# Performance work log

Measured on AMD Instinct MI355X. Metric: run time of the kernel, lower is better.

## Reference

```python
import jax, jax.numpy as jnp
import numpy as np
import math

B, S_TGT, S_SRC, D, H, FF = 4, 2048, 2048, 512, 8, 2048
DK = D // H
EPS = 1e-6


def layernorm(x, gamma, mu):
    # torch: gamma*(x-mean)/(std+eps)+mu with unbiased std (ddof=1), eps OUTSIDE sqrt
    mean = jnp.mean(x, axis=-1, keepdims=True)
    std = jnp.std(x, axis=-1, keepdims=True, ddof=1)
    return gamma * (x - mean) / (std + EPS) + mu


def mha(q, k, v, wq, wk, wv, wo, bo, mask):
    # q:[B,Sq,D] k,v:[B,Sk,D]; weights [D,D] (applied as x@W)
    Bq, Sq, _ = q.shape
    Sk = k.shape[1]
    Q = (q @ wq).reshape(Bq, Sq, H, DK).transpose(0, 2, 1, 3)  # [B,H,Sq,dk]
    K = (k @ wk).reshape(Bq, Sk, H, DK).transpose(0, 2, 1, 3)
    V = (v @ wv).reshape(Bq, Sk, H, DK).transpose(0, 2, 1, 3)
    scores = jnp.einsum('bhqd,bhkd->bhqk', Q, K) / math.sqrt(DK)
    scores = jnp.where(mask == 0, -1e9, scores)
    attn = jax.nn.softmax(scores, axis=-1)
    out = jnp.einsum('bhqk,bhkd->bhqd', attn, V)  # [B,H,Sq,dk]
    out = out.transpose(0, 2, 1, 3).reshape(Bq, Sq, D)
    return out @ wo + bo


def setup_inputs() -> dict:
    key = jax.random.key(0)
    ks = jax.random.split(key, 20)
    sc = 0.02
    inp = {
        'x': jax.random.normal(ks[0], (B, S_TGT, D), jnp.float32),
        'encoder_output': jax.random.normal(ks[1], (B, S_SRC, D), jnp.float32),
        'src_mask': jnp.ones((1, 1, 1, S_SRC), jnp.int32),
        'tgt_mask': jnp.tril(jnp.ones((S_TGT, S_TGT), jnp.int32))[None, None],
        # self-attention params
        'sa_wq': jax.random.normal(ks[2], (D, D)) * sc,
        'sa_wk': jax.random.normal(ks[3], (D, D)) * sc,
        'sa_wv': jax.random.normal(ks[4], (D, D)) * sc,
        'sa_wo': jax.random.normal(ks[5], (D, D)) * sc,
        'sa_bo': jnp.zeros((D,), jnp.float32),
        # cross-attention params
        'ca_wq': jax.random.normal(ks[6], (D, D)) * sc,
        'ca_wk': jax.random.normal(ks[7], (D, D)) * sc,
        'ca_wv': jax.random.normal(ks[8], (D, D)) * sc,
        'ca_wo': jax.random.normal(ks[9], (D, D)) * sc,
        'ca_bo': jnp.zeros((D,), jnp.float32),
        # feed-forward params
        'ff_w1': jax.random.normal(ks[10], (D, FF)) * sc,
        'ff_b1': jnp.zeros((FF,), jnp.float32),
        'ff_w2': jax.random.normal(ks[11], (FF, D)) * sc,
        'ff_b2': jnp.zeros((D,), jnp.float32),
        # layernorm params (3 residual connections)
        'ln0_g': jnp.ones((D,), jnp.float32), 'ln0_b': jnp.zeros((D,), jnp.float32),
        'ln1_g': jnp.ones((D,), jnp.float32), 'ln1_b': jnp.zeros((D,), jnp.float32),
        'ln2_g': jnp.ones((D,), jnp.float32), 'ln2_b': jnp.zeros((D,), jnp.float32),
    }
    return inp


def reference(x, encoder_output, src_mask, tgt_mask,
              sa_wq, sa_wk, sa_wv, sa_wo, sa_bo,
              ca_wq, ca_wk, ca_wv, ca_wo, ca_bo,
              ff_w1, ff_b1, ff_w2, ff_b2,
              ln0_g, ln0_b, ln1_g, ln1_b, ln2_g, ln2_b):
    # pre-LN residual blocks; dropout in eval mode (identity)
    h = layernorm(x, ln0_g, ln0_b)
    x = x + mha(h, h, h, sa_wq, sa_wk, sa_wv, sa_wo, sa_bo, tgt_mask)
    h = layernorm(x, ln1_g, ln1_b)
    x = x + mha(h, encoder_output, encoder_output, ca_wq, ca_wk, ca_wv, ca_wo, ca_bo, src_mask)
    h = layernorm(x, ln2_g, ln2_b)
    ff = jax.nn.relu(h @ ff_w1 + ff_b1) @ ff_w2 + ff_b2
    return x + ff
```

## Files before the change

### kernel.cpp

```cpp
#include <hip/hip_runtime.h>
#include <cstdint>

typedef short s8v __attribute__((ext_vector_type(8)));
typedef short s4v __attribute__((ext_vector_type(4)));
typedef float f4v __attribute__((ext_vector_type(4)));
typedef unsigned int u32;

#define DEV static __device__ __forceinline__

DEV unsigned short f2bf(float f) {
  u32 u = __builtin_bit_cast(u32, f);
  u += 0x7FFF + ((u >> 16) & 1);
  return (unsigned short)(u >> 16);
}

DEV void gload16(const void* g, void* l) {
  __builtin_amdgcn_global_load_lds(
      (const __attribute__((address_space(1))) u32*)g,
      (__attribute__((address_space(3))) u32*)l, 16, 0, 0);
}

struct TransArgs {
  const float* in[10];
  unsigned short* out[10];
};

__global__ __launch_bounds__(256) void trans_all_kernel(TransArgs ta) {
  int id = blockIdx.x;
  int wi, t, K, N, tx, ty;
  if (id < 2048) {
    wi = id >> 8; t = id & 255; K = 512; N = 512; tx = t & 15; ty = t >> 4;
  } else if (id < 3072) {
    wi = 8; t = id - 2048; K = 512; N = 2048; tx = t & 63; ty = t >> 6;
  } else {
    wi = 9; t = id - 3072; K = 2048; N = 512; tx = t & 15; ty = t >> 4;
  }
  const float* in = ta.in[wi];
  unsigned short* out = ta.out[wi];
  __shared__ float tile[32][33];
  int lx = threadIdx.x & 31, ly = threadIdx.x >> 5;
  int bn = tx * 32, bk = ty * 32;
#pragma unroll
  for (int i = 0; i < 32; i += 8)
    tile[ly + i][lx] = in[(size_t)(bk + ly + i) * N + bn + lx];
  __syncthreads();
#pragma unroll
  for (int i = 0; i < 32; i += 8)
    out[(size_t)(bn + ly + i) * K + bk + lx] = f2bf(tile[lx][ly + i]);
}

__global__ __launch_bounds__(256) void cast_kernel(
    const float* __restrict__ in, unsigned short* __restrict__ out, int n8) {
  int i = blockIdx.x * 256 + threadIdx.x;
  if (i >= n8) return;
  const float4* p = (const float4*)(in + (size_t)i * 8);
  float4 a = p[0], b = p[1];
  float va[8] = {a.x, a.y, a.z, a.w, b.x, b.y, b.z, b.w};
  s8v o;
#pragma unroll
  for (int j = 0; j < 8; j++) o[j] = (short)f2bf(va[j]);
  *(s8v*)(out + (size_t)i * 8) = o;
}

__global__ __launch_bounds__(256) void ln_kernel(
    const float* __restrict__ x, const float* __restrict__ g,
    const float* __restrict__ bt, unsigned short* __restrict__ out) {
  int row = blockIdx.x * 4 + (threadIdx.x >> 6);
  int lane = threadIdx.x & 63;
  const float* xr = x + (size_t)row * 512 + lane * 8;
  float4 v0 = *(const float4*)xr;
  float4 v1 = *(const float4*)(xr + 4);
  float va[8] = {v0.x, v0.y, v0.z, v0.w, v1.x, v1.y, v1.z, v1.w};
  float s = 0.f, s2 = 0.f;
#pragma unroll
  for (int j = 0; j < 8; j++) { s += va[j]; s2 += va[j] * va[j]; }
#pragma unroll
  for (int off = 1; off < 64; off <<= 1) {
    s += __shfl_xor(s, off);
    s2 += __shfl_xor(s2, off);
  }
  float mean = s * (1.f / 512.f);
  float var = (s2 - 512.f * mean * mean) * (1.f / 511.f);
  var = fmaxf(var, 0.f);
  float inv = 1.f / (sqrtf(var) + 1e-6f);
  const float* gp = g + lane * 8;
  const float* bp = bt + lane * 8;
  float4 g0 = *(const float4*)gp, g1 = *(const float4*)(gp + 4);
  float4 b0 = *(const float4*)bp, b1 = *(const float4*)(bp + 4);
  float ga[8] = {g0.x, g0.y, g0.z, g0.w, g1.x, g1.y, g1.z, g1.w};
  float ba[8] = {b0.x, b0.y, b0.z, b0.w, b1.x, b1.y, b1.z, b1.w};
  s8v o;
#pragma unroll
  for (int j = 0; j < 8; j++)
    o[j] = (short)f2bf(ga[j] * (va[j] - mean) * inv + ba[j]);
  *(s8v*)(out + (size_t)row * 512 + lane * 8) = o;
}

#define EPI_QKV3 0
#define EPI_Q 1
#define EPI_KV2 2
#define EPI_BIAS_RES 3
#define EPI_RELU 4

template <int EPI>
__global__ __launch_bounds__(256) void gemm_kernel(
    const unsigned short* __restrict__ A, const unsigned short* __restrict__ Bt,
    const float* __restrict__ bias, const float* __restrict__ res,
    void* __restrict__ out0, void* __restrict__ out1, void* __restrict__ out2,
    int M, int N, int K) {
  __shared__ alignas(16) unsigned short sA[128 * 32];
  __shared__ alignas(16) unsigned short sB[128 * 32];
  int tid = threadIdx.x;
  int w = tid >> 6, lane = tid & 63;
  int wm = w >> 1, wn = w & 1;
  int quad = lane >> 4, l15 = lane & 15;
  int bm = blockIdx.y * 128, bn = blockIdx.x * 128;

  int r0 = lane >> 2, c0 = (lane & 3) * 8;
  const unsigned short* gA0 = A + (size_t)(bm + w * 16 + r0) * K + c0;
  const unsigned short* gA1 = gA0 + (size_t)64 * K;
  const unsigned short* gB0 = Bt + (size_t)(bn + w * 16 + r0) * K + c0;
  const unsigned short* gB1 = gB0 + (size_t)64 * K;
  unsigned short* lA0 = &sA[(w * 64 + lane) * 8];
  unsigned short* lA1 = &sA[((w + 4) * 64 + lane) * 8];
  unsigned short* lB0 = &sB[(w * 64 + lane) * 8];
  unsigned short* lB1 = &sB[((w + 4) * 64 + lane) * 8];

  f4v acc[4][4];
#pragma unroll
  for (int r = 0; r < 4; r++)
#pragma unroll
    for (int c = 0; c < 4; c++) acc[r][c] = {0.f, 0.f, 0.f, 0.f};

  for (int k0 = 0; k0 < K; k0 += 32) {
    gload16(gA0 + k0, lA0);
    gload16(gA1 + k0, lA1);
    gload16(gB0 + k0, lB0);
    gload16(gB1 + k0, lB1);
    __syncthreads();
    s8v af[4], bf[4];
#pragma unroll
    for (int r = 0; r < 4; r++)
      af[r] = *(const s8v*)&sA[(wm * 64 + r * 16 + l15) * 32 + quad * 8];
#pragma unroll
    for (int c = 0; c < 4; c++)
      bf[c] = *(const s8v*)&sB[(wn * 64 + c * 16 + l15) * 32 + quad * 8];
#pragma unroll
    for (int r = 0; r < 4; r++)
#pragma unroll
      for (int c = 0; c < 4; c++)
        acc[r][c] = __builtin_amdgcn_mfma_f32_16x16x32_bf16(af[r], bf[c], acc[r][c], 0, 0, 0);
    __syncthreads();
  }

  int route = 0;
  if (EPI == EPI_QKV3) route = blockIdx.x >> 2;
  if (EPI == EPI_KV2) route = 1 + (blockIdx.x >> 2);
#pragma unroll
  for (int r = 0; r < 4; r++) {
#pragma unroll
    for (int c = 0; c < 4; c++) {
#pragma unroll
      for (int i = 0; i < 4; i++) {
        int row = bm + wm * 64 + r * 16 + quad * 4 + i;
        int col = bn + wn * 64 + c * 16 + l15;
        float v = acc[r][c][i];
        if (EPI == EPI_BIAS_RES) {
          float* o = (float*)out0;
          o[(size_t)row * N + col] = v + bias[col] + res[(size_t)row * N + col];
        } else if (EPI == EPI_RELU) {
          unsigned short* o = (unsigned short*)out0;
          o[(size_t)row * N + col] = f2bf(fmaxf(v + bias[col], 0.f));
        } else {
          int colq = col & 511;
          int b = row >> 11, s = row & 2047, h = colq >> 6, dk = colq & 63;
          if (route == 0) {
            unsigned short* o = (unsigned short*)out0;
            o[(((size_t)(b * 8 + h) * 2048) + s) * 64 + dk] = f2bf(v * 0.125f);
          } else if (route == 1) {
            unsigned short* o = (unsigned short*)out1;
            o[(((size_t)(b * 8 + h) * 2048) + s) * 64 + dk] = f2bf(v);
          } else {
            unsigned short* o = (unsigned short*)out2;
            o[(((size_t)(b * 8 + h) * 64) + dk) * 2048 + s] = f2bf(v);
          }
        }
      }
    }
  }
}

template <int CAUSAL>
__global__ __launch_bounds__(256, 4) void attn_kernel(
    const unsigned short* __restrict__ Q, const unsigned short* __restrict__ Kk,
    const unsigned short* __restrict__ Vt,
    unsigned short* __restrict__ out) {
  const int S = 2048;
  __shared__ alignas(16) unsigned short sK[64 * 64];
  __shared__ alignas(16) unsigned short sV[64 * 64];
  __shared__ alignas(16) unsigned short sO[64 * 68];
  int bh = blockIdx.x;
  int qt = CAUSAL ? ((int)gridDim.y - 1 - blockIdx.y) : blockIdx.y;
  int b = bh >> 3, h = bh & 7;
  int tid = threadIdx.x;
  int w = tid >> 6, lane = tid & 63;
  int quad = lane >> 4, l15 = lane & 15;

  const unsigned short* Qp = Q + (size_t)bh * S * 64;
  const unsigned short* Kp = Kk + (size_t)bh * S * 64;
  const unsigned short* Vp = Vt + (size_t)bh * 64 * S;

  s8v bq[2];
  {
    const unsigned short* qr = Qp + (size_t)(qt * 64 + w * 16 + l15) * 64 + quad * 8;
    bq[0] = *(const s8v*)qr;
    bq[1] = *(const s8v*)(qr + 32);
  }

  int rowA = ((l15 >> 2) * 8) + (l15 & 3);
  int koff[2][2][2];
#pragma unroll
  for (int win = 0; win < 2; win++)
#pragma unroll
    for (int half = 0; half < 2; half++) {
      int row = win * 32 + half * 4 + rowA;
      int h7 = (row & 7) ^ (((row >> 3) & 1) << 2);
      koff[win][half][0] = row * 64 + ((quad ^ h7) << 3);
      koff[win][half][1] = row * 64 + (((4 + quad) ^ h7) << 3);
    }
  int voff[4][2];
#pragma unroll
  for (int c2 = 0; c2 < 4; c2++) {
    int row = c2 * 16 + l15;
    int h7 = (row & 7) ^ (((row >> 3) & 1) << 2);
#pragma unroll
    for (int win = 0; win < 2; win++)
      voff[c2][win] = row * 64 + ((((win * 4) + quad) ^ h7) << 3);
  }
  int st_row[2], st_lds[2], st_cc[2];
#pragma unroll
  for (int c = 0; c < 2; c++) {
    int row = c * 32 + (tid >> 3), cc = tid & 7;
    int slot = cc ^ (row & 7) ^ (((row >> 3) & 1) << 2);
    st_row[c] = row;
    st_cc[c] = cc;
    st_lds[c] = row * 64 + slot * 8;
  }

  float l_lane = 0.f;
  f4v oacc[4];
#pragma unroll
  for (int c2 = 0; c2 < 4; c2++) oacc[c2] = {0.f, 0.f, 0.f, 0.f};

  int ntiles = CAUSAL ? (qt + 1) : (S / 64);
  for (int t = 0; t < ntiles; t++) {
    int kb = t * 64;
    __syncthreads();
#pragma unroll
    for (int c = 0; c < 2; c++) {
      *(s8v*)&sK[st_lds[c]] = *(const s8v*)(Kp + (size_t)(kb + st_row[c]) * 64 + st_cc[c] * 8);
      *(s8v*)&sV[st_lds[c]] = *(const s8v*)(Vp + (size_t)st_row[c] * S + kb + st_cc[c] * 8);
    }
    __syncthreads();

    f4v sacc[2][2];
#pragma unroll
    for (int win = 0; win < 2; win++)
#pragma unroll
      for (int half = 0; half < 2; half++) {
        sacc[win][half] = {0.f, 0.f, 0.f, 0.f};
        s8v a0 = *(const s8v*)&sK[koff[win][half][0]];
        s8v a1 = *(const s8v*)&sK[koff[win][half][1]];
        sacc[win][half] = __builtin_amdgcn_mfma_f32_16x16x32_bf16(a0, bq[0], sacc[win][half], 0, 0, 0);
        sacc[win][half] = __builtin_amdgcn_mfma_f32_16x16x32_bf16(a1, bq[1], sacc[win][half], 0, 0, 0);
      }

    if (CAUSAL && t == qt) {
      int qloc = w * 16 + l15;
#pragma unroll
      for (int win = 0; win < 2; win++)
#pragma unroll
        for (int half = 0; half < 2; half++)
#pragma unroll
          for (int i = 0; i < 4; i++)
            if (win * 32 + quad * 8 + half * 4 + i > qloc) sacc[win][half][i] = -1e9f;
    }

    s8v bp[2];
#pragma unroll
    for (int win = 0; win < 2; win++) {
      float p[8];
#pragma unroll
      for (int half = 0; half < 2; half++)
#pragma unroll
        for (int i = 0; i < 4; i++) {
          float e = __expf(sacc[win][half][i]);
          p[half * 4 + i] = e;
          l_lane += e;
        }
      int4 pk;
#pragma unroll
      for (int j = 0; j < 4; j++)
        pk[j] = (int)__builtin_amdgcn_perm(
            __builtin_bit_cast(u32, p[2 * j + 1]),
            __builtin_bit_cast(u32, p[2 * j]), 0x07060302u);
      bp[win] = __builtin_bit_cast(s8v, pk);
    }

#pragma unroll
    for (int c2 = 0; c2 < 4; c2++)
#pragma unroll
      for (int win = 0; win < 2; win++) {
        s8v av = *(const s8v*)&sV[voff[c2][win]];
        oacc[c2] = __builtin_amdgcn_mfma_f32_16x16x32_bf16(av, bp[win], oacc[c2], 0, 0, 0);
      }
  }

  float l = l_lane;
  l += __shfl_xor(l, 16);
  l += __shfl_xor(l, 32);
  float inv = 1.f / l;
#pragma unroll
  for (int c2 = 0; c2 < 4; c2++) {
    s4v o;
#pragma unroll
    for (int i = 0; i < 4; i++) o[i] = (short)f2bf(oacc[c2][i] * inv);
    *(s4v*)&sO[(w * 16 + l15) * 68 + c2 * 16 + quad * 4] = o;
  }
  __syncthreads();
#pragma unroll
  for (int c = 0; c < 2; c++) {
    int idx = c * 256 + tid;
    int r = idx >> 3, ch = idx & 7;
    s8v v = *(const s8v*)&sO[r * 68 + ch * 8];
    *(s8v*)(out + ((size_t)(b * S + qt * 64 + r) * 512) + h * 64 + ch * 8) = v;
  }
}

extern "C" void kernel_launch(void* const* d_in, const int* in_sizes, int n_in,
                              void* d_out, int out_size, void* d_ws, size_t ws_size,
                              hipStream_t stream) {
  const float* x = (const float*)d_in[0];
  const float* enc = (const float*)d_in[1];
  const float* sa_wq = (const float*)d_in[4];
  const float* sa_wk = (const float*)d_in[5];
  const float* sa_wv = (const float*)d_in[6];
  const float* sa_wo = (const float*)d_in[7];
  const float* sa_bo = (const float*)d_in[8];
  const float* ca_wq = (const float*)d_in[9];
  const float* ca_wk = (const float*)d_in[10];
  const float* ca_wv = (const float*)d_in[11];
  const float* ca_wo = (const float*)d_in[12];
  const float* ca_bo = (const float*)d_in[13];
  const float* ff_w1 = (const float*)d_in[14];
  const float* ff_b1 = (const float*)d_in[15];
  const float* ff_w2 = (const float*)d_in[16];
  const float* ff_b2 = (const float*)d_in[17];
  const float* ln0_g = (const float*)d_in[18];
  const float* ln0_b = (const float*)d_in[19];
  const float* ln1_g = (const float*)d_in[20];
  const float* ln1_b = (const float*)d_in[21];
  const float* ln2_g = (const float*)d_in[22];
  const float* ln2_b = (const float*)d_in[23];
  float* out = (float*)d_out;

  const int M = 8192;

  size_t off = 0;
  auto carve = [&](size_t bytes) -> void* {
    void* r = (char*)d_ws + off;
    off += (bytes + 255) & ~(size_t)255;
    return r;
  };
  unsigned short* swqT = (unsigned short*)carve(512 * 512 * 2);
  unsigned short* swkT = (unsigned short*)carve(512 * 512 * 2);
  unsigned short* swvT = (unsigned short*)carve(512 * 512 * 2);
  unsigned short* swoT = (unsigned short*)carve(512 * 512 * 2);
  unsigned short* cwqT = (unsigned short*)carve(512 * 512 * 2);
  unsigned short* cwkT = (unsigned short*)carve(512 * 512 * 2);
  unsigned short* cwvT = (unsigned short*)carve(512 * 512 * 2);
  unsigned short* cwoT = (unsigned short*)carve(512 * 512 * 2);
  unsigned short* w1T = (unsigned short*)carve((size_t)2048 * 512 * 2);
  unsigned short* w2T = (unsigned short*)carve((size_t)512 * 2048 * 2);
  unsigned short* enc_bf = (unsigned short*)carve((size_t)M * 512 * 2);
  unsigned short* h_bf = (unsigned short*)carve((size_t)M * 512 * 2);
  unsigned short* Qb = (unsigned short*)carve((size_t)M * 512 * 2);
  unsigned short* Kb = (unsigned short*)carve((size_t)M * 512 * 2);
  unsigned short* Vtb = (unsigned short*)carve((size_t)M * 512 * 2);
  unsigned short* attn_bf = (unsigned short*)carve((size_t)M * 512 * 2);
  float* x1 = (float*)carve((size_t)M * 512 * 4);
  unsigned short* f1 = (unsigned short*)carve((size_t)M * 2048 * 2);

  dim3 blk(256);

  TransArgs ta;
  ta.in[0] = sa_wq; ta.out[0] = swqT;
  ta.in[1] = sa_wk; ta.out[1] = swkT;
  ta.in[2] = sa_wv; ta.out[2] = swvT;
  ta.in[3] = sa_wo; ta.out[3] = swoT;
  ta.in[4] = ca_wq; ta.out[4] = cwqT;
  ta.in[5] = ca_wk; ta.out[5] = cwkT;
  ta.in[6] = ca_wv; ta.out[6] = cwvT;
  ta.in[7] = ca_wo; ta.out[7] = cwoT;
  ta.in[8] = ff_w1; ta.out[8] = w1T;
  ta.in[9] = ff_w2; ta.out[9] = w2T;
  trans_all_kernel<<<dim3(4096), blk, 0, stream>>>(ta);
  cast_kernel<<<dim3(M * 512 / 8 / 256), blk, 0, stream>>>(enc, enc_bf, M * 512 / 8);

  dim3 gProj(4, 64);
  dim3 gQKV(12, 64);
  dim3 gKV(8, 64);
  dim3 gFF1(16, 64);
  dim3 gAttn(32, 32);
  dim3 gLN(M / 4);

  ln_kernel<<<gLN, blk, 0, stream>>>(x, ln0_g, ln0_b, h_bf);
  gemm_kernel<EPI_QKV3><<<gQKV, blk, 0, stream>>>(h_bf, swqT, nullptr, nullptr, Qb, Kb, Vtb, M, 1536, 512);
  attn_kernel<1><<<gAttn, blk, 0, stream>>>(Qb, Kb, Vtb, attn_bf);
  gemm_kernel<EPI_BIAS_RES><<<gProj, blk, 0, stream>>>(attn_bf, swoT, sa_bo, x, x1, nullptr, nullptr, M, 512, 512);

  ln_kernel<<<gLN, blk, 0, stream>>>(x1, ln1_g, ln1_b, h_bf);
  gemm_kernel<EPI_Q><<<gProj, blk, 0, stream>>>(h_bf, cwqT, nullptr, nullptr, Qb, nullptr, nullptr, M, 512, 512);
  gemm_kernel<EPI_KV2><<<gKV, blk, 0, stream>>>(enc_bf, cwkT, nullptr, nullptr, nullptr, Kb, Vtb, M, 1024, 512);
  attn_kernel<0><<<gAttn, blk, 0, stream>>>(Qb, Kb, Vtb, attn_bf);
  gemm_kernel<EPI_BIAS_RES><<<gProj, blk, 0, stream>>>(attn_bf, cwoT, ca_bo, x1, x1, nullptr, nullptr, M, 512, 512);

  ln_kernel<<<gLN, blk, 0, stream>>>(x1, ln2_g, ln2_b, h_bf);
  gemm_kernel<EPI_RELU><<<gFF1, blk, 0, stream>>>(h_bf, w1T, ff_b1, nullptr, f1, nullptr, nullptr, M, 2048, 512);
  gemm_kernel<EPI_BIAS_RES><<<gProj, blk, 0, stream>>>(f1, w2T, ff_b2, x1, out, nullptr, nullptr, M, 512, 2048);
}
```

Baseline: 447.4 us.

## Double-buffer GEMM and attention tiles, widen attention Q tile, narrow GEMM N tile

After: 415.6 us. 7.1% less time.

```diff
diff --git a/kernel.cpp b/kernel.cpp
--- a/kernel.cpp
+++ b/kernel.cpp
@@ -102,68 +102,72 @@
 #define EPI_BIAS_RES 3
 #define EPI_RELU 4
 
-template <int EPI>
-__global__ __launch_bounds__(256) void gemm_kernel(
+template <int EPI, int BN>
+__global__ __launch_bounds__(256, 3) void gemm_kernel(
     const unsigned short* __restrict__ A, const unsigned short* __restrict__ Bt,
     const float* __restrict__ bias, const float* __restrict__ res,
     void* __restrict__ out0, void* __restrict__ out1, void* __restrict__ out2,
     int M, int N, int K) {
-  __shared__ alignas(16) unsigned short sA[128 * 32];
-  __shared__ alignas(16) unsigned short sB[128 * 32];
+  __shared__ alignas(16) unsigned short sA[2][128 * 32];
+  __shared__ alignas(16) unsigned short sB[2][BN * 32];
+  constexpr int NC = BN / 32;
   int tid = threadIdx.x;
   int w = tid >> 6, lane = tid & 63;
   int wm = w >> 1, wn = w & 1;
   int quad = lane >> 4, l15 = lane & 15;
-  int bm = blockIdx.y * 128, bn = blockIdx.x * 128;
+  int bm = blockIdx.y * 128, bn = blockIdx.x * BN;
 
   int r0 = lane >> 2, c0 = (lane & 3) * 8;
   const unsigned short* gA0 = A + (size_t)(bm + w * 16 + r0) * K + c0;
   const unsigned short* gA1 = gA0 + (size_t)64 * K;
   const unsigned short* gB0 = Bt + (size_t)(bn + w * 16 + r0) * K + c0;
   const unsigned short* gB1 = gB0 + (size_t)64 * K;
-  unsigned short* lA0 = &sA[(w * 64 + lane) * 8];
-  unsigned short* lA1 = &sA[((w + 4) * 64 + lane) * 8];
-  unsigned short* lB0 = &sB[(w * 64 + lane) * 8];
-  unsigned short* lB1 = &sB[((w + 4) * 64 + lane) * 8];
-
-  f4v acc[4][4];
+
+  auto prefetch = [&](int k0, int buf) {
+    gload16(gA0 + k0, &sA[buf][w * 512]);
+    gload16(gA1 + k0, &sA[buf][(w + 4) * 512]);
+    gload16(gB0 + k0, &sB[buf][w * 512]);
+    if (BN == 128) gload16(gB1 + k0, &sB[buf][(w + 4) * 512]);
+  };
+
+  f4v acc[4][NC];
 #pragma unroll
   for (int r = 0; r < 4; r++)
 #pragma unroll
-    for (int c = 0; c < 4; c++) acc[r][c] = {0.f, 0.f, 0.f, 0.f};
-
-  for (int k0 = 0; k0 < K; k0 += 32) {
-    gload16(gA0 + k0, lA0);
-    gload16(gA1 + k0, lA1);
-    gload16(gB0 + k0, lB0);
-    gload16(gB1 + k0, lB1);
+    for (int c = 0; c < NC; c++) acc[r][c] = {0.f, 0.f, 0.f, 0.f};
+
+  prefetch(0, 0);
+  int nk = K >> 5;
+  for (int it = 0; it < nk; it++) {
+    int buf = it & 1;
     __syncthreads();
-    s8v af[4], bf[4];
+    if (it + 1 < nk) prefetch((it + 1) << 5, buf ^ 1);
+    s8v af[4], bf[NC];
 #pragma unroll
     for (int r = 0; r < 4; r++)
-      af[r] = *(const s8v*)&sA[(wm * 64 + r * 16 + l15) * 32 + quad * 8];
-#pragma unroll
-    for (int c = 0; c < 4; c++)
-      bf[c] = *(const s8v*)&sB[(wn * 64 + c * 16 + l15) * 32 + quad * 8];
+      af[r] = *(const s8v*)&sA[buf][(wm * 64 + r * 16 + l15) * 32 + quad * 8];
+#pragma unroll
+    for (int c = 0; c < NC; c++)
+      bf[c] = *(const s8v*)&sB[buf][(wn * (BN / 2) + c * 16 + l15) * 32 + quad * 8];
 #pragma unroll
     for (int r = 0; r < 4; r++)
 #pragma unroll
-      for (int c = 0; c < 4; c++)
+      for (int c = 0; c < NC; c++)
         acc[r][c] = __builtin_amdgcn_mfma_f32_16x16x32_bf16(af[r], bf[c], acc[r][c], 0, 0, 0);
-    __syncthreads();
-  }
-
+  }
+
+  constexpr int BP = 512 / BN;
   int route = 0;
-  if (EPI == EPI_QKV3) route = blockIdx.x >> 2;
-  if (EPI == EPI_KV2) route = 1 + (blockIdx.x >> 2);
+  if (EPI == EPI_QKV3) route = blockIdx.x / BP;
+  if (EPI == EPI_KV2) route = 1 + blockIdx.x / BP;
 #pragma unroll
   for (int r = 0; r < 4; r++) {
 #pragma unroll
-    for (int c = 0; c < 4; c++) {
+    for (int c = 0; c < NC; c++) {
 #pragma unroll
       for (int i = 0; i < 4; i++) {
         int row = bm + wm * 64 + r * 16 + quad * 4 + i;
-        int col = bn + wn * 64 + c * 16 + l15;
+        int col = bn + wn * (BN / 2) + c * 16 + l15;
         float v = acc[r][c][i];
         if (EPI == EPI_BIAS_RES) {
           float* o = (float*)out0;
@@ -191,14 +195,14 @@
 }
 
 template <int CAUSAL>
-__global__ __launch_bounds__(256, 4) void attn_kernel(
+__global__ __launch_bounds__(256, 2) void attn_kernel(
     const unsigned short* __restrict__ Q, const unsigned short* __restrict__ Kk,
     const unsigned short* __restrict__ Vt,
     unsigned short* __restrict__ out) {
   const int S = 2048;
-  __shared__ alignas(16) unsigned short sK[64 * 64];
-  __shared__ alignas(16) unsigned short sV[64 * 64];
-  __shared__ alignas(16) unsigned short sO[64 * 68];
+  __shared__ alignas(16) unsigned short sK[2][64 * 64];
+  __shared__ alignas(16) unsigned short sV[2][64 * 64];
+  __shared__ alignas(16) unsigned short sO[128 * 68];
   int bh = blockIdx.x;
   int qt = CAUSAL ? ((int)gridDim.y - 1 - blockIdx.y) : blockIdx.y;
   int b = bh >> 3, h = bh & 7;
@@ -210,11 +214,13 @@
   const unsigned short* Kp = Kk + (size_t)bh * S * 64;
   const unsigned short* Vp = Vt + (size_t)bh * 64 * S;
 
-  s8v bq[2];
-  {
-    const unsigned short* qr = Qp + (size_t)(qt * 64 + w * 16 + l15) * 64 + quad * 8;
-    bq[0] = *(const s8v*)qr;
-    bq[1] = *(const s8v*)(qr + 32);
+  s8v bq[2][2];
+#pragma unroll
+  for (int qb = 0; qb < 2; qb++) {
+    const unsigned short* qr =
+        Qp + (size_t)(qt * 128 + w * 32 + qb * 16 + l15) * 64 + quad * 8;
+    bq[qb][0] = *(const s8v*)qr;
+    bq[qb][1] = *(const s8v*)(qr + 32);
   }
 
   int rowA = ((l15 >> 2) * 8) + (l15 & 3);
@@ -247,93 +253,136 @@
     st_lds[c] = row * 64 + slot * 8;
   }
 
-  float l_lane = 0.f;
-  f4v oacc[4];
-#pragma unroll
-  for (int c2 = 0; c2 < 4; c2++) oacc[c2] = {0.f, 0.f, 0.f, 0.f};
-
-  int ntiles = CAUSAL ? (qt + 1) : (S / 64);
+  float l_lane[2] = {0.f, 0.f};
+  f4v oacc[2][4];
+#pragma unroll
+  for (int qb = 0; qb < 2; qb++)
+#pragma unroll
+    for (int c2 = 0; c2 < 4; c2++) oacc[qb][c2] = {0.f, 0.f, 0.f, 0.f};
+
+  int ntiles = CAUSAL ? (2 * qt + 2) : (S / 64);
+
+  s8v kreg[2], vreg[2];
+  auto load_t = [&](int t) {
+    int kb = t * 64;
+#pragma unroll
+    for (int c = 0; c < 2; c++) {
+      kreg[c] = *(const s8v*)(Kp + (size_t)(kb + st_row[c]) * 64 + st_cc[c] * 8);
+      vreg[c] = *(const s8v*)(Vp + (size_t)st_row[c] * S + kb + st_cc[c] * 8);
+    }
+  };
+  auto write_t = [&](int buf) {
+#pragma unroll
+    for (int c = 0; c < 2; c++) {
+      *(s8v*)&sK[buf][st_lds[c]] = kreg[c];
+      *(s8v*)&sV[buf][st_lds[c]] = vreg[c];
+    }
+  };
+
+  load_t(0);
+  write_t(0);
+
   for (int t = 0; t < ntiles; t++) {
-    int kb = t * 64;
+    int buf = t & 1;
     __syncthreads();
-#pragma unroll
-    for (int c = 0; c < 2; c++) {
-      *(s8v*)&sK[st_lds[c]] = *(const s8v*)(Kp + (size_t)(kb + st_row[c]) * 64 + st_cc[c] * 8);
-      *(s8v*)&sV[st_lds[c]] = *(const s8v*)(Vp + (size_t)st_row[c] * S + kb + st_cc[c] * 8);
-    }
-    __syncthreads();
-
-    f4v sacc[2][2];
+    if (t + 1 < ntiles) load_t(t + 1);
+
+    f4v sacc[2][2][2];
+#pragma unroll
+    for (int qb = 0; qb < 2; qb++)
+#pragma unroll
+      for (int win = 0; win < 2; win++)
+#pragma unroll
+        for (int half = 0; half < 2; half++) sacc[qb][win][half] = {0.f, 0.f, 0.f, 0.f};
 #pragma unroll
     for (int win = 0; win < 2; win++)
 #pragma unroll
       for (int half = 0; half < 2; half++) {
-        sacc[win][half] = {0.f, 0.f, 0.f, 0.f};
-        s8v a0 = *(const s8v*)&sK[koff[win][half][0]];
-        s8v a1 = *(const s8v*)&sK[koff[win][half][1]];
-        sacc[win][half] = __builtin_amdgcn_mfma_f32_16x16x32_bf16(a0, bq[0], sacc[win][half], 0, 0, 0);
-        sacc[win][half] = __builtin_amdgcn_mfma_f32_16x16x32_bf16(a1, bq[1], sacc[win][half], 0, 0, 0);
+        s8v a0 = *(const s8v*)&sK[buf][koff[win][half][0]];
+        s8v a1 = *(const s8v*)&sK[buf][koff[win][half][1]];
+#pragma unroll
+        for (int qb = 0; qb < 2; qb++) {
+          sacc[qb][win][half] =
+              __builtin_amdgcn_mfma_f32_16x16x32_bf16(a0, bq[qb][0], sacc[qb][win][half], 0, 0, 0);
+          sacc[qb][win][half] =
+              __builtin_amdgcn_mfma_f32_16x16x32_bf16(a1, bq[qb][1], sacc[qb][win][half], 0, 0, 0);
+        }
       }
 
-    if (CAUSAL && t == qt) {
-      int qloc = w * 16 + l15;
-#pragma unroll
-      for (int win = 0; win < 2; win++)
+    if (CAUSAL && t >= 2 * qt) {
+      int toff = (t - 2 * qt) * 64;
+#pragma unroll
+      for (int qb = 0; qb < 2; qb++) {
+        int qloc = w * 32 + qb * 16 + l15;
+#pragma unroll
+        for (int win = 0; win < 2; win++)
+#pragma unroll
+          for (int half = 0; half < 2; half++)
+#pragma unroll
+            for (int i = 0; i < 4; i++)
+              if (toff + win * 32 + quad * 8 + half * 4 + i > qloc)
+                sacc[qb][win][half][i] = -1e9f;
+      }
+    }
+
+    s8v bp[2][2];
+#pragma unroll
+    for (int qb = 0; qb < 2; qb++)
+#pragma unroll
+      for (int win = 0; win < 2; win++) {
+        float p[8];
 #pragma unroll
         for (int half = 0; half < 2; half++)
 #pragma unroll
-          for (int i = 0; i < 4; i++)
-            if (win * 32 + quad * 8 + half * 4 + i > qloc) sacc[win][half][i] = -1e9f;
-    }
-
-    s8v bp[2];
-#pragma unroll
-    for (int win = 0; win < 2; win++) {
-      float p[8];
-#pragma unroll
-      for (int half = 0; half < 2; half++)
-#pragma unroll
-        for (int i = 0; i < 4; i++) {
-          float e = __expf(sacc[win][half][i]);
-          p[half * 4 + i] = e;
-          l_lane += e;
-        }
-      int4 pk;
-#pragma unroll
-      for (int j = 0; j < 4; j++)
-        pk[j] = (int)__builtin_amdgcn_perm(
-            __builtin_bit_cast(u32, p[2 * j + 1]),
-            __builtin_bit_cast(u32, p[2 * j]), 0x07060302u);
-      bp[win] = __builtin_bit_cast(s8v, pk);
-    }
+          for (int i = 0; i < 4; i++) {
+            float e = __expf(sacc[qb][win][half][i]);
+            p[half * 4 + i] = e;
+            l_lane[qb] += e;
+          }
+        int4 pk;
+#pragma unroll
+        for (int j = 0; j < 4; j++)
+          pk[j] = (int)__builtin_amdgcn_perm(
+              __builtin_bit_cast(u32, p[2 * j + 1]),
+              __builtin_bit_cast(u32, p[2 * j]), 0x07060302u);
+        bp[qb][win] = __builtin_bit_cast(s8v, pk);
+      }
 
 #pragma unroll
     for (int c2 = 0; c2 < 4; c2++)
 #pragma unroll
       for (int win = 0; win < 2; win++) {
-        s8v av = *(const s8v*)&sV[voff[c2][win]];
-        oacc[c2] = __builtin_amdgcn_mfma_f32_16x16x32_bf16(av, bp[win], oacc[c2], 0, 0, 0);
+        s8v av = *(const s8v*)&sV[buf][voff[c2][win]];
+#pragma unroll
+        for (int qb = 0; qb < 2; qb++)
+          oacc[qb][c2] =
+              __builtin_amdgcn_mfma_f32_16x16x32_bf16(av, bp[qb][win], oacc[qb][c2], 0, 0, 0);
       }
-  }
-
-  float l = l_lane;
-  l += __shfl_xor(l, 16);
-  l += __shfl_xor(l, 32);
-  float inv = 1.f / l;
-#pragma unroll
-  for (int c2 = 0; c2 < 4; c2++) {
-    s4v o;
-#pragma unroll
-    for (int i = 0; i < 4; i++) o[i] = (short)f2bf(oacc[c2][i] * inv);
-    *(s4v*)&sO[(w * 16 + l15) * 68 + c2 * 16 + quad * 4] = o;
+
+    if (t + 1 < ntiles) write_t(buf ^ 1);
+  }
+
+#pragma unroll
+  for (int qb = 0; qb < 2; qb++) {
+    float l = l_lane[qb];
+    l += __shfl_xor(l, 16);
+    l += __shfl_xor(l, 32);
+    float inv = 1.f / l;
+#pragma unroll
+    for (int c2 = 0; c2 < 4; c2++) {
+      s4v o;
+#pragma unroll
+      for (int i = 0; i < 4; i++) o[i] = (short)f2bf(oacc[qb][c2][i] * inv);
+      *(s4v*)&sO[(w * 32 + qb * 16 + l15) * 68 + c2 * 16 + quad * 4] = o;
+    }
   }
   __syncthreads();
 #pragma unroll
-  for (int c = 0; c < 2; c++) {
+  for (int c = 0; c < 4; c++) {
     int idx = c * 256 + tid;
     int r = idx >> 3, ch = idx & 7;
     s8v v = *(const s8v*)&sO[r * 68 + ch * 8];
-    *(s8v*)(out + ((size_t)(b * S + qt * 64 + r) * 512) + h * 64 + ch * 8) = v;
+    *(s8v*)(out + ((size_t)(b * S + qt * 128 + r) * 512) + h * 64 + ch * 8) = v;
   }
 }
 
@@ -407,25 +456,25 @@
   trans_all_kernel<<<dim3(4096), blk, 0, stream>>>(ta);
   cast_kernel<<<dim3(M * 512 / 8 / 256), blk, 0, stream>>>(enc, enc_bf, M * 512 / 8);
 
-  dim3 gProj(4, 64);
+  dim3 gProj(8, 64);
   dim3 gQKV(12, 64);
-  dim3 gKV(8, 64);
+  dim3 gKV(16, 64);
   dim3 gFF1(16, 64);
-  dim3 gAttn(32, 32);
+  dim3 gAttn(32, 16);
   dim3 gLN(M / 4);
 
   ln_kernel<<<gLN, blk, 0, stream>>>(x, ln0_g, ln0_b, h_bf);
-  gemm_kernel<EPI_QKV3><<<gQKV, blk, 0, stream>>>(h_bf, swqT, nullptr, nullptr, Qb, Kb, Vtb, M, 1536, 512);
+  gemm_kernel<EPI_QKV3, 128><<<gQKV, blk, 0, stream>>>(h_bf, swqT, nullptr, nullptr, Qb, Kb, Vtb, M, 1536, 512);
   attn_kernel<1><<<gAttn, blk, 0, stream>>>(Qb, Kb, Vtb, attn_bf);
-  gemm_kernel<EPI_BIAS_RES><<<gProj, blk, 0, stream>>>(attn_bf, swoT, sa_bo, x, x1, nullptr, nullptr, M, 512, 512);
+  gemm_kernel<EPI_BIAS_RES, 64><<<gProj, blk, 0, stream>>>(attn_bf, swoT, sa_bo, x, x1, nullptr, nullptr, M, 512, 512);
 
   ln_kernel<<<gLN, blk, 0, stream>>>(x1, ln1_g, ln1_b, h_bf);
-  gemm_kernel<EPI_Q><<<gProj, blk, 0, stream>>>(h_bf, cwqT, nullptr, nullptr, Qb, nullptr, nullptr, M, 512, 512);
-  gemm_kernel<EPI_KV2><<<gKV, blk, 0, stream>>>(enc_bf, cwkT, nullptr, nullptr, nullptr, Kb, Vtb, M, 1024, 512);
+  gemm_kernel<EPI_Q, 64><<<gProj, blk, 0, stream>>>(h_bf, cwqT, nullptr, nullptr, Qb, nullptr, nullptr, M, 512, 512);
+  gemm_kernel<EPI_KV2, 64><<<gKV, blk, 0, stream>>>(enc_bf, cwkT, nullptr, nullptr, nullptr, Kb, Vtb, M, 1024, 512);
   attn_kernel<0><<<gAttn, blk, 0, stream>>>(Qb, Kb, Vtb, attn_bf);
-  gemm_kernel<EPI_BIAS_RES><<<gProj, blk, 0, stream>>>(attn_bf, cwoT, ca_bo, x1, x1, nullptr, nullptr, M, 512, 512);
+  gemm_kernel<EPI_BIAS_RES, 64><<<gProj, blk, 0, stream>>>(attn_bf, cwoT, ca_bo, x1, x1, nullptr, nullptr, M, 512, 512);
 
   ln_kernel<<<gLN, blk, 0, stream>>>(x1, ln2_g, ln2_b, h_bf);
-  gemm_kernel<EPI_RELU><<<gFF1, blk, 0, stream>>>(h_bf, w1T, ff_b1, nullptr, f1, nullptr, nullptr, M, 2048, 512);
-  gemm_kernel<EPI_BIAS_RES><<<gProj, blk, 0, stream>>>(f1, w2T, ff_b2, x1, out, nullptr, nullptr, M, 512, 2048);
-}
+  gemm_kernel<EPI_RELU, 128><<<gFF1, blk, 0, stream>>>(h_bf, w1T, ff_b1, nullptr, f1, nullptr, nullptr, M, 2048, 512);
+  gemm_kernel<EPI_BIAS_RES, 64><<<gProj, blk, 0, stream>>>(f1, w2T, ff_b2, x1, out, nullptr, nullptr, M, 512, 2048);
+}
```
